# Performance work log

Hardware: AMD Instinct MI355X
Metric: run time of the kernel (lower is better)

Reference implementation:

```python
import jax, jax.numpy as jnp
import numpy as np

MARGIN = 1.0  # from init_kwargs
B, H, W, P = 64, 512, 640, 100000


def setup_inputs() -> dict:
    key = jax.random.key(0)
    k0, k1, k2, k3, k4, k5 = jax.random.split(key, 6)
    return {
        "inp": jax.random.normal(k0, (B, 1, H, W), dtype=jnp.float32),
        "x_A": jax.random.randint(k1, (B, P), 0, W, dtype=jnp.int32),
        "y_A": jax.random.randint(k2, (B, P), 0, H, dtype=jnp.int32),
        "x_B": jax.random.randint(k3, (B, P), 0, W, dtype=jnp.int32),
        "y_B": jax.random.randint(k4, (B, P), 0, H, dtype=jnp.int32),
        "ordinal": jax.random.randint(k5, (B, P), 0, 3, dtype=jnp.int32),
    }


def reference(inp, x_A, y_A, x_B, y_B, ordinal):
    # inp: [B,1,H,W]; point coords: [B,P]; ordinal in {0,1,2} -> gt in {-1,0,1}
    depth = inp[:, 0]                                   # [B,H,W]
    bidx = jnp.arange(depth.shape[0])[:, None]          # [B,1]
    z_A = depth[bidx, y_A, x_A]                         # [B,P] gather
    z_B = depth[bidx, y_B, x_B]                         # [B,P] gather
    gt = (ordinal - 1).astype(depth.dtype)              # {-1,0,1}
    mask = jnp.abs(gt)
    zd = z_A - z_B
    m = jnp.asarray(MARGIN, depth.dtype)
    # ordered pairs: log(1+exp(-min(gt*zd, m))); equal pairs: max(zd^2, m^2)
    loss = mask * jnp.log(1.0 + jnp.exp(-jnp.minimum(gt * zd, m))) \
         + (1.0 - mask) * jnp.maximum(zd * zd, m * m)
    n_point_total = depth.shape[0] * x_A.shape[1]
    return jnp.sum(loss) / n_point_total
```

## Files before the change

kernel.cpp:

```cpp
#include <hip/hip_runtime.h>


constexpr int B = 64;
constexpr int H = 512;
constexpr int W = 640;
constexpr int P = 100000;
constexpr int N4 = (B * P) / 4;
constexpr float INV_N = 1.0f / (float)(B * P);
constexpr float MARGIN = 1.0f;

__device__ __forceinline__ float loss_elem(const float* __restrict__ d,
                                           int ya, int xa, int yb, int xb, int od) {
    float za = d[ya * W + xa];
    float zb = d[yb * W + xb];
    float zd = za - zb;
    float gt = (float)(od - 1);
    float mask = fabsf(gt);
    float t = fminf(gt * zd, MARGIN);
    float l_rank = __logf(1.0f + __expf(-t));
    float l_eq = fmaxf(zd * zd, MARGIN * MARGIN);
    return mask * l_rank + (1.0f - mask) * l_eq;
}

__global__ __launch_bounds__(256) void rdc_kernel(
        const float* __restrict__ depth,
        const int4* __restrict__ xA, const int4* __restrict__ yA,
        const int4* __restrict__ xB, const int4* __restrict__ yB,
        const int4* __restrict__ ord,
        float* __restrict__ out) {
    int i = blockIdx.x * blockDim.x + threadIdx.x;
    float acc = 0.0f;
    if (i < N4) {
        int b = i / (P / 4);
        const float* d = depth + (size_t)b * (H * W);
        int4 xa = xA[i], ya = yA[i], xb = xB[i], yb = yB[i], od = ord[i];
        acc += loss_elem(d, ya.x, xa.x, yb.x, xb.x, od.x);
        acc += loss_elem(d, ya.y, xa.y, yb.y, xb.y, od.y);
        acc += loss_elem(d, ya.z, xa.z, yb.z, xb.z, od.z);
        acc += loss_elem(d, ya.w, xa.w, yb.w, xb.w, od.w);
    }

    #pragma unroll
    for (int off = 32; off > 0; off >>= 1)
        acc += __shfl_down(acc, off, 64);

    __shared__ float wsum[4];
    int lane = threadIdx.x & 63;
    int wid  = threadIdx.x >> 6;
    if (lane == 0) wsum[wid] = acc;
    __syncthreads();
    if (wid == 0) {
        float v = (lane < 4) ? wsum[lane] : 0.0f;
        #pragma unroll
        for (int off = 2; off > 0; off >>= 1)
            v += __shfl_down(v, off, 64);
        if (lane == 0)
            atomicAdd(out, v * INV_N);
    }
}

extern "C" void kernel_launch(void* const* d_in, const int* in_sizes, int n_in,
                              void* d_out, int out_size, void* d_ws, size_t ws_size,
                              hipStream_t stream) {
    const float* depth = (const float*)d_in[0];
    const int4* xA = (const int4*)d_in[1];
    const int4* yA = (const int4*)d_in[2];
    const int4* xB = (const int4*)d_in[3];
    const int4* yB = (const int4*)d_in[4];
    const int4* ord = (const int4*)d_in[5];
    float* out = (float*)d_out;

    hipMemsetAsync(out, 0, sizeof(float), stream);

    int blocks = (N4 + 255) / 256;
    rdc_kernel<<<blocks, 256, 0, stream>>>(depth, xA, yA, xB, yB, ord, out);
}
```

Baseline: 277.0 us.

## Interleave batch blocks across XCDs, use nontemporal loads and two-pass reduction

```diff
diff --git a/kernel.cpp b/kernel.cpp
--- a/kernel.cpp
+++ b/kernel.cpp
@@ -5,9 +5,13 @@
 constexpr int H = 512;
 constexpr int W = 640;
 constexpr int P = 100000;
-constexpr int N4 = (B * P) / 4;
+constexpr int N4B = P / 4;
+constexpr int CHUNKS = (N4B + 255) / 256;
+constexpr int NBLK = B * CHUNKS;
 constexpr float INV_N = 1.0f / (float)(B * P);
 constexpr float MARGIN = 1.0f;
+
+typedef int vint4 __attribute__((ext_vector_type(4)));
 
 __device__ __forceinline__ float loss_elem(const float* __restrict__ d,
                                            int ya, int xa, int yb, int xb, int od) {
@@ -24,16 +28,26 @@
 
 __global__ __launch_bounds__(256) void rdc_kernel(
         const float* __restrict__ depth,
-        const int4* __restrict__ xA, const int4* __restrict__ yA,
-        const int4* __restrict__ xB, const int4* __restrict__ yB,
-        const int4* __restrict__ ord,
-        float* __restrict__ out) {
-    int i = blockIdx.x * blockDim.x + threadIdx.x;
+        const vint4* __restrict__ xA, const vint4* __restrict__ yA,
+        const vint4* __restrict__ xB, const vint4* __restrict__ yB,
+        const vint4* __restrict__ ord,
+        float* __restrict__ partials) {
+    int j = blockIdx.x;
+    int x = j & 7;
+    int g = j >> 3;
+    int b = ((g / CHUNKS) << 3) + x;
+    int c = g % CHUNKS;
+    int e = c * 256 + threadIdx.x;
+
     float acc = 0.0f;
-    if (i < N4) {
-        int b = i / (P / 4);
+    if (e < N4B) {
+        int i = b * N4B + e;
         const float* d = depth + (size_t)b * (H * W);
-        int4 xa = xA[i], ya = yA[i], xb = xB[i], yb = yB[i], od = ord[i];
+        vint4 xa = __builtin_nontemporal_load(&xA[i]);
+        vint4 ya = __builtin_nontemporal_load(&yA[i]);
+        vint4 xb = __builtin_nontemporal_load(&xB[i]);
+        vint4 yb = __builtin_nontemporal_load(&yB[i]);
+        vint4 od = __builtin_nontemporal_load(&ord[i]);
         acc += loss_elem(d, ya.x, xa.x, yb.x, xb.x, od.x);
         acc += loss_elem(d, ya.y, xa.y, yb.y, xb.y, od.y);
         acc += loss_elem(d, ya.z, xa.z, yb.z, xb.z, od.z);
@@ -49,29 +63,82 @@
     int wid  = threadIdx.x >> 6;
     if (lane == 0) wsum[wid] = acc;
     __syncthreads();
-    if (wid == 0) {
-        float v = (lane < 4) ? wsum[lane] : 0.0f;
-        #pragma unroll
-        for (int off = 2; off > 0; off >>= 1)
-            v += __shfl_down(v, off, 64);
-        if (lane == 0)
-            atomicAdd(out, v * INV_N);
+    if (wid == 0 && lane == 0) {
+        partials[j] = wsum[0] + wsum[1] + wsum[2] + wsum[3];
     }
+}
+
+__global__ __launch_bounds__(256) void rdc_finalize(
+        const float* __restrict__ partials, float* __restrict__ out, int n) {
+    float acc = 0.0f;
+    for (int k = threadIdx.x; k < n; k += 256)
+        acc += partials[k];
+    #pragma unroll
+    for (int off = 32; off > 0; off >>= 1)
+        acc += __shfl_down(acc, off, 64);
+    __shared__ float wsum[4];
+    int lane = threadIdx.x & 63;
+    int wid  = threadIdx.x >> 6;
+    if (lane == 0) wsum[wid] = acc;
+    __syncthreads();
+    if (wid == 0 && lane == 0)
+        out[0] = (wsum[0] + wsum[1] + wsum[2] + wsum[3]) * INV_N;
+}
+
+__global__ __launch_bounds__(256) void rdc_kernel_atomic(
+        const float* __restrict__ depth,
+        const vint4* __restrict__ xA, const vint4* __restrict__ yA,
+        const vint4* __restrict__ xB, const vint4* __restrict__ yB,
+        const vint4* __restrict__ ord,
+        float* __restrict__ out) {
+    int j = blockIdx.x;
+    int x = j & 7, g = j >> 3;
+    int b = ((g / CHUNKS) << 3) + x;
+    int c = g % CHUNKS;
+    int e = c * 256 + threadIdx.x;
+    float acc = 0.0f;
+    if (e < N4B) {
+        int i = b * N4B + e;
+        const float* d = depth + (size_t)b * (H * W);
+        vint4 xa = __builtin_nontemporal_load(&xA[i]);
+        vint4 ya = __builtin_nontemporal_load(&yA[i]);
+        vint4 xb = __builtin_nontemporal_load(&xB[i]);
+        vint4 yb = __builtin_nontemporal_load(&yB[i]);
+        vint4 od = __builtin_nontemporal_load(&ord[i]);
+        acc += loss_elem(d, ya.x, xa.x, yb.x, xb.x, od.x);
+        acc += loss_elem(d, ya.y, xa.y, yb.y, xb.y, od.y);
+        acc += loss_elem(d, ya.z, xa.z, yb.z, xb.z, od.z);
+        acc += loss_elem(d, ya.w, xa.w, yb.w, xb.w, od.w);
+    }
+    #pragma unroll
+    for (int off = 32; off > 0; off >>= 1)
+        acc += __shfl_down(acc, off, 64);
+    __shared__ float wsum[4];
+    int lane = threadIdx.x & 63;
+    int wid  = threadIdx.x >> 6;
+    if (lane == 0) wsum[wid] = acc;
+    __syncthreads();
+    if (wid == 0 && lane == 0)
+        atomicAdd(out, (wsum[0] + wsum[1] + wsum[2] + wsum[3]) * INV_N);
 }
 
 extern "C" void kernel_launch(void* const* d_in, const int* in_sizes, int n_in,
                               void* d_out, int out_size, void* d_ws, size_t ws_size,
                               hipStream_t stream) {
     const float* depth = (const float*)d_in[0];
-    const int4* xA = (const int4*)d_in[1];
-    const int4* yA = (const int4*)d_in[2];
-    const int4* xB = (const int4*)d_in[3];
-    const int4* yB = (const int4*)d_in[4];
-    const int4* ord = (const int4*)d_in[5];
+    const vint4* xA = (const vint4*)d_in[1];
+    const vint4* yA = (const vint4*)d_in[2];
+    const vint4* xB = (const vint4*)d_in[3];
+    const vint4* yB = (const vint4*)d_in[4];
+    const vint4* ord = (const vint4*)d_in[5];
     float* out = (float*)d_out;
 
-    hipMemsetAsync(out, 0, sizeof(float), stream);
-
-    int blocks = (N4 + 255) / 256;
-    rdc_kernel<<<blocks, 256, 0, stream>>>(depth, xA, yA, xB, yB, ord, out);
+    if (ws_size >= NBLK * sizeof(float)) {
+        float* partials = (float*)d_ws;
+        rdc_kernel<<<NBLK, 256, 0, stream>>>(depth, xA, yA, xB, yB, ord, partials);
+        rdc_finalize<<<1, 256, 0, stream>>>(partials, out, NBLK);
+    } else {
+        hipMemsetAsync(out, 0, sizeof(float), stream);
+        rdc_kernel_atomic<<<NBLK, 256, 0, stream>>>(depth, xA, yA, xB, yB, ord, out);
+    }
 }
```

New measurement: 243.7 us. 12.0% less time.
